# Kernel optimization log

Hardware: AMD Instinct MI355X
Metric: run time of the kernel (lower is better)

Reference implementation:

```python
import jax, jax.numpy as jnp
import numpy as np

N = 50000
E = 640000
IN_DIM = 23
HID = 128
NUM_CLASS = 12


def setup_inputs() -> dict:
    key = jax.random.key(0)
    ks = jax.random.split(key, 12)
    x = jax.random.normal(ks[0], (N, IN_DIM), dtype=jnp.float32)
    edge_index = jax.random.randint(ks[1], (2, E), 0, N, dtype=jnp.int32)

    def glorot(k, shape):
        fan_in, fan_out = shape
        lim = np.sqrt(6.0 / (fan_in + fan_out)).astype(np.float32)
        return jax.random.uniform(k, shape, jnp.float32, -lim, lim)

    W1 = glorot(ks[2], (IN_DIM, HID)); b1 = jnp.zeros((HID,), jnp.float32)
    W2 = glorot(ks[3], (HID, HID));    b2 = jnp.zeros((HID,), jnp.float32)
    W3 = glorot(ks[4], (HID, HID));    b3 = jnp.zeros((HID,), jnp.float32)
    Wc1 = glorot(ks[5], (HID, 64));    bc1 = jnp.zeros((64,), jnp.float32)
    Wc2 = glorot(ks[6], (64, NUM_CLASS)); bc2 = jnp.zeros((NUM_CLASS,), jnp.float32)
    return {"x": x, "edge_index": edge_index,
            "W1": W1, "b1": b1, "W2": W2, "b2": b2, "W3": W3, "b3": b3,
            "Wc1": Wc1, "bc1": bc1, "Wc2": Wc2, "bc2": bc2}


def _gcn_norm(edge_index, n_nodes):
    # add self loops, compute symmetric normalization D^-1/2 (A+I) D^-1/2
    loop = jnp.arange(n_nodes, dtype=edge_index.dtype)
    src = jnp.concatenate([edge_index[0], loop])
    dst = jnp.concatenate([edge_index[1], loop])
    deg = jax.ops.segment_sum(jnp.ones_like(dst, dtype=jnp.float32), dst,
                              num_segments=n_nodes)
    dinv = jax.lax.rsqrt(deg)  # deg >= 1 due to self loops
    norm = dinv[src] * dinv[dst]  # [E + N]
    return src, dst, norm


def _gcn_layer(h, W, b, src, dst, norm, n_nodes):
    h = h @ W                          # linear (bias applied after aggregation, per PyG)
    msg = h[src] * norm[:, None]       # gather + scale
    out = jax.ops.segment_sum(msg, dst, num_segments=n_nodes)  # scatter-add
    return out + b


def reference(x, edge_index, W1, b1, W2, b2, W3, b3, Wc1, bc1, Wc2, bc2):
    n = x.shape[0]
    src, dst, norm = _gcn_norm(edge_index, n)
    h = jnp.tanh(_gcn_layer(x, W1, b1, src, dst, norm, n))
    h = jnp.tanh(_gcn_layer(h, W2, b2, src, dst, norm, n))
    h = jnp.tanh(_gcn_layer(h, W3, b3, src, dst, norm, n))
    # dropout is identity in eval mode
    out = h @ Wc1 + bc1
    out = out @ Wc2 + bc2
    return out
```

## Files before the change

kernel.cpp:

```cpp
#include <hip/hip_runtime.h>
#include <math.h>

#define NN 50000
#define EE 640000
#define IND 23
#define HID 128
#define MIDD 64
#define NCLS 12
#define NB 49
#define QS 32766.0f
#define INVQS (1.0f / 32766.0f)
#define BSH 7
#define NBK 391
#define CHUNK 4096
#define NPB 157
#define PADB 6250
#define GB16 3125

typedef short short8v __attribute__((ext_vector_type(8)));
typedef float f32x4 __attribute__((ext_vector_type(4)));
typedef unsigned long long u64;

__device__ __forceinline__ short f2bf(float f) {
    unsigned u = __float_as_uint(f);
    unsigned r = (u + 0x7FFFu + ((u >> 16) & 1u)) >> 16;
    return (short)r;
}
__device__ __forceinline__ float bf2f(short s) {
    return __uint_as_float(((unsigned)(unsigned short)s) << 16);
}
__device__ __forceinline__ float fast_tanh(float x) {
    float t = __expf(-2.f * fabsf(x));
    float r = (1.f - t) / (1.f + t);
    return copysignf(r, x);
}

__global__ __launch_bounds__(256) void k_pre(const int* __restrict__ dst,
                                             int* __restrict__ cnt,
                                             const float* __restrict__ Wc1,
                                             const float* __restrict__ bc1,
                                             const float* __restrict__ Wc2,
                                             const float* __restrict__ bc2,
                                             float* __restrict__ Wcc,
                                             float* __restrict__ bcc,
                                             const float* __restrict__ W2,
                                             const float* __restrict__ W3,
                                             short* __restrict__ w2hi,
                                             short* __restrict__ w2lo,
                                             short* __restrict__ w3hi,
                                             short* __restrict__ w3lo) {
    const int bid = blockIdx.x;
    const int tid = threadIdx.x;
    if (bid < 2500) {
        int i = bid * 256 + tid;
        if (i < EE) atomicAdd(&cnt[dst[i]], 1);
        return;
    }
    if (bid < 2506) {
        int t = (bid - 2500) * 256 + tid;
        if (t < HID * NCLS) {
            int k = t / NCLS, c = t % NCLS;
            float s = 0.f;
#pragma unroll 8
            for (int j = 0; j < MIDD; ++j) s += Wc1[k * MIDD + j] * Wc2[j * NCLS + c];
            Wcc[t] = s;
        }
        if (t < NCLS) {
            float s = bc2[t];
#pragma unroll 8
            for (int j = 0; j < MIDD; ++j) s += bc1[j] * Wc2[j * NCLS + t];
            bcc[t] = s;
        }
        return;
    }
    int bb = bid - 2506;
    const float* W = (bb < 64) ? W2 : W3;
    short* hi = (bb < 64) ? w2hi : w3hi;
    short* lo = (bb < 64) ? w2lo : w3lo;
    int i = (bb & 63) * 256 + tid;
    int k = i >> 7, c = i & 127;
    float w = W[i];
    short h = f2bf(w);
    short l = f2bf(w - bf2f(h));
    hi[((k >> 3) * 128 + c) * 8 + (k & 7)] = h;
    lo[((k >> 3) * 128 + c) * 8 + (k & 7)] = l;
}

__global__ __launch_bounds__(256) void k_scan_local(const int* __restrict__ cnt,
                                                    int* __restrict__ row_ptr,
                                                    float* __restrict__ dinv,
                                                    int* __restrict__ sums) {
    __shared__ int wtot[4];
    const int tid = threadIdx.x;
    const int wid = tid >> 6, lane = tid & 63;
    const int base = blockIdx.x * 1024 + tid * 4;
    int v[4];
#pragma unroll
    for (int t = 0; t < 4; ++t) {
        int i = base + t;
        v[t] = (i < NN) ? cnt[i] : 0;
        if (i < NN) dinv[i] = rsqrtf((float)v[t] + 1.0f);
    }
    int slocal = v[0] + v[1] + v[2] + v[3];
    int val = slocal;
#pragma unroll
    for (int off = 1; off < 64; off <<= 1) {
        int t = __shfl_up(val, off, 64);
        if (lane >= off) val += t;
    }
    if (lane == 63) wtot[wid] = val;
    __syncthreads();
    int woff = 0;
#pragma unroll
    for (int w = 0; w < 4; ++w) woff += (w < wid) ? wtot[w] : 0;
    int run = woff + val - slocal;
#pragma unroll
    for (int t = 0; t < 4; ++t) {
        int i = base + t;
        if (i < NN) row_ptr[i] = run;
        run += v[t];
    }
    if (tid == 255) sums[blockIdx.x] = woff + val;
}

__global__ __launch_bounds__(256) void k_scan_apply2(int* __restrict__ row_ptr,
                                                     const int* __restrict__ sums,
                                                     int* __restrict__ bcurA) {
    __shared__ int so;
    const int tid = threadIdx.x;
    if (tid < 64) {
        int a = (tid < (int)blockIdx.x) ? sums[tid] : 0;
        int b = (tid < NB) ? sums[tid] : 0;
#pragma unroll
        for (int off = 32; off; off >>= 1) {
            a += __shfl_down(a, off, 64);
            b += __shfl_down(b, off, 64);
        }
        if (tid == 0) {
            so = a;
            if (blockIdx.x == NB - 1) row_ptr[NN] = b;
        }
    }
    __syncthreads();
    const int o = so;
    const int base = blockIdx.x * 1024 + tid * 4;
#pragma unroll
    for (int t = 0; t < 4; ++t) {
        int i = base + t;
        if (i < NN) {
            int rp = row_ptr[i] + o;
            row_ptr[i] = rp;
            if ((i & 127) == 0) bcurA[i >> BSH] = rp;
        }
    }
}

__global__ __launch_bounds__(256) void k_part(const int* __restrict__ src,
                                              const int* __restrict__ dst,
                                              const float* __restrict__ dinv,
                                              int* __restrict__ bcurA,
                                              u64* __restrict__ sw_g,
                                              int* __restrict__ d_g,
                                              const float* __restrict__ x,
                                              float* __restrict__ xp) {
    const int bid = blockIdx.x;
    const int tid = threadIdx.x;
    if (bid >= NPB) {
        int i = (bid - NPB) * 256 + tid;
        int node = i >> 5, f = i & 31;
        xp[i] = (f < IND) ? x[node * IND + f] * dinv[node] : 0.f;
        return;
    }
    __shared__ int hist[NBK], base[NBK], cur[NBK], gb[NBK];
    __shared__ u64 lsw[CHUNK];
    __shared__ int ld[CHUNK];
    const int e0 = bid * CHUNK;
    const int total = min(CHUNK, EE - e0);
    for (int t = tid; t < NBK; t += 256) hist[t] = 0;
    __syncthreads();
    int sv[16], dv[16];
#pragma unroll
    for (int t = 0; t < 16; ++t) {
        int i = e0 + t * 256 + tid;
        if (i < EE) {
            sv[t] = src[i];
            dv[t] = dst[i];
            atomicAdd(&hist[dv[t] >> BSH], 1);
        } else dv[t] = -1;
    }
    __syncthreads();
    if (tid < 64) {
        int carry = 0;
        for (int c = 0; c < NBK; c += 64) {
            int idx = c + tid;
            int v = (idx < NBK) ? hist[idx] : 0;
            int sc = v;
#pragma unroll
            for (int off = 1; off < 64; off <<= 1) {
                int tv = __shfl_up(sc, off, 64);
                if (tid >= off) sc += tv;
            }
            if (idx < NBK) base[idx] = carry + sc - v;
            carry += __shfl(sc, 63, 64);
        }
    }
    __syncthreads();
    for (int t = tid; t < NBK; t += 256) {
        cur[t] = base[t];
        gb[t] = hist[t] ? atomicAdd(&bcurA[t], hist[t]) : 0;
    }
    __syncthreads();
#pragma unroll
    for (int t = 0; t < 16; ++t) {
        if (dv[t] >= 0) {
            int b = dv[t] >> BSH;
            int r = atomicAdd(&cur[b], 1);
            lsw[r] = (unsigned)sv[t] |
                     ((u64)__float_as_uint(dinv[sv[t]]) << 32);
            ld[r] = dv[t];
        }
    }
    __syncthreads();
    for (int j = tid; j < total; j += 256) {
        int d = ld[j];
        int b = d >> BSH;
        int gpos = gb[b] + (j - base[b]);
        sw_g[gpos] = lsw[j];
        d_g[gpos] = d;
    }
}

__global__ __launch_bounds__(256) void k_sort(const int* __restrict__ row_ptr,
                                              const u64* __restrict__ sw_g,
                                              const int* __restrict__ d_g,
                                              u64* __restrict__ e_sn) {
    __shared__ int rloc[129];
    __shared__ int curl[128];
    __shared__ u64 osw[3072];
    const int bid = blockIdx.x, tid = threadIdx.x;
    const int n0 = bid << BSH;
    const int nlast = min(128, NN - n0);
    if (tid <= nlast) rloc[tid] = row_ptr[n0 + tid];
    if (tid < 128) curl[tid] = 0;
    __syncthreads();
    const int rbeg = rloc[0];
    const int cnt = rloc[nlast] - rbeg;
    for (int j = tid; j < cnt; j += 256) {
        int d = d_g[rbeg + j];
        int li = d - n0;
        int r = atomicAdd(&curl[li], 1);
        int pl = (rloc[li] - rbeg) + r;
        u64 v = sw_g[rbeg + j];
        if (pl < 3072) osw[pl] = v;
        else e_sn[rbeg + pl] = v;
    }
    __syncthreads();
    const int lim = min(cnt, 3072);
    for (int j = tid; j < lim; j += 256) e_sn[rbeg + j] = osw[j];
}

__global__ __launch_bounds__(256) void k_l1(const float* __restrict__ xp,
                                            const float* __restrict__ W1,
                                            const float* __restrict__ b1,
                                            const int* __restrict__ row_ptr,
                                            const int2* __restrict__ e_sn,
                                            const float* __restrict__ dinv,
                                            short* __restrict__ outq) {
    const int tid = threadIdx.x;
    const int i = blockIdx.x * 4 + (tid >> 6);
    const int lane = tid & 63;
    const int slot = lane >> 3;
    const int f = lane & 7;
    const float4* xp4 = (const float4*)xp;
    const int beg = row_ptr[i];
    const int deg = row_ptr[i + 1] - beg;
    float4 acc = make_float4(0.f, 0.f, 0.f, 0.f);
    for (int base = 0; base < deg; base += 64) {
        const int cnt = min(64, deg - base);
        int s_l = 0;
        if (lane < cnt) s_l = e_sn[beg + base + lane].x;
        int e = 0;
        for (; e + 8 <= cnt; e += 8) {
            int s = __shfl(s_l, e + slot, 64);
            float4 v = xp4[s * 8 + f];
            acc.x += v.x; acc.y += v.y; acc.z += v.z; acc.w += v.w;
        }
        if (e < cnt) {
            int s = __shfl(s_l, e + slot, 64);
            if (e + slot < cnt) {
                float4 v = xp4[s * 8 + f];
                acc.x += v.x; acc.y += v.y; acc.z += v.z; acc.w += v.w;
            }
        }
    }
#pragma unroll
    for (int off = 32; off >= 8; off >>= 1) {
        acc.x += __shfl_down(acc.x, off, 64);
        acc.y += __shfl_down(acc.y, off, 64);
        acc.z += __shfl_down(acc.z, off, 64);
        acc.w += __shfl_down(acc.w, off, 64);
    }
    const float di = dinv[i];
    if (lane < 8) {
        float4 v = xp4[i * 8 + lane];
        acc.x = (acc.x + v.x) * di; acc.y = (acc.y + v.y) * di;
        acc.z = (acc.z + v.z) * di; acc.w = (acc.w + v.w) * di;
    }
    float a0 = b1[lane], a1 = b1[lane + 64];
#pragma unroll
    for (int k = 0; k < IND; ++k) {
        float comp = ((k & 3) == 0) ? acc.x : ((k & 3) == 1) ? acc.y
                   : ((k & 3) == 2) ? acc.z : acc.w;
        float xk = __shfl(comp, k >> 2, 64);
        a0 += xk * W1[k * HID + lane];
        a1 += xk * W1[k * HID + lane + 64];
    }
    outq[i * HID + lane]      = (short)__float2int_rn(fast_tanh(a0) * QS);
    outq[i * HID + lane + 64] = (short)__float2int_rn(fast_tanh(a1) * QS);
}

__global__ __launch_bounds__(256) void k_aggq(const short* __restrict__ hq,
                                              const int* __restrict__ row_ptr,
                                              const int2* __restrict__ e_sn,
                                              const float* __restrict__ dinv,
                                              short8v* __restrict__ ah,
                                              short8v* __restrict__ al) {
    const int tid = threadIdx.x;
    const int i = blockIdx.x * 4 + (tid >> 6);
    const int lane = tid & 63;
    const int slot = lane >> 4;
    const int f = lane & 15;
    const short8v* h8 = (const short8v*)hq;
    const int beg = row_ptr[i];
    const int deg = row_ptr[i + 1] - beg;
    float facc[8];
#pragma unroll
    for (int t = 0; t < 8; ++t) facc[t] = 0.f;
    for (int base = 0; base < deg; base += 64) {
        const int cnt = min(64, deg - base);
        int s_l = 0; float n_l = 0.f;
        if (lane < cnt) {
            int2 sn = e_sn[beg + base + lane];
            s_l = sn.x;
            n_l = __int_as_float(sn.y);
        }
        int e = 0;
#pragma unroll 4
        for (; e + 4 <= cnt; e += 4) {
            int s = __shfl(s_l, e + slot, 64);
            float nr = __shfl(n_l, e + slot, 64);
            short8v v = h8[(size_t)s * 16 + f];
#pragma unroll
            for (int t = 0; t < 8; ++t) facc[t] += (float)v[t] * nr;
        }
        if (e < cnt) {
            int s = __shfl(s_l, e + slot, 64);
            float nr = __shfl(n_l, e + slot, 64);
            if (e + slot < cnt) {
                short8v v = h8[(size_t)s * 16 + f];
#pragma unroll
                for (int t = 0; t < 8; ++t) facc[t] += (float)v[t] * nr;
            }
        }
    }
#pragma unroll
    for (int off = 32; off >= 16; off >>= 1)
#pragma unroll
        for (int t = 0; t < 8; ++t) facc[t] += __shfl_down(facc[t], off, 64);
    if (lane < 16) {
        const float di = dinv[i];
        const float sc = di * INVQS;
        short8v v = h8[(size_t)i * 16 + lane];
        short8v hi8, lo8;
#pragma unroll
        for (int t = 0; t < 8; ++t) {
            float o = (facc[t] + di * (float)v[t]) * sc;
            short h = f2bf(o);
            hi8[t] = h;
            lo8[t] = f2bf(o - bf2f(h));
        }
        ah[(size_t)i * 16 + lane] = hi8;
        al[(size_t)i * 16 + lane] = lo8;
    }
}

#define GEMM_CORE16                                                            \
    const int tid = threadIdx.x;                                               \
    const int lane = tid & 63, wv = tid >> 6;                                  \
    const int g = lane >> 4, c16 = lane & 15;                                  \
    const int rb = blockIdx.x * 16;                                            \
    const int colb = wv * 32;                                                  \
    const size_t arow = (size_t)(rb + c16) * 16;                               \
    short8v Ah[4], Al[4], Bh[4][2], Bl[4][2];                                  \
    _Pragma("unroll")                                                          \
    for (int t = 0; t < 4; ++t) {                                              \
        Ah[t] = ah[arow + t * 4 + g];                                          \
        Al[t] = al[arow + t * 4 + g];                                          \
        _Pragma("unroll")                                                      \
        for (int ct = 0; ct < 2; ++ct) {                                       \
            int wi = (t * 4 + g) * 128 + colb + ct * 16 + c16;                 \
            Bh[t][ct] = whi8[wi];                                              \
            Bl[t][ct] = wlo8[wi];                                              \
        }                                                                      \
    }                                                                          \
    __builtin_amdgcn_sched_barrier(0);                                         \
    f32x4 acc[2];                                                              \
    acc[0] = f32x4{0.f, 0.f, 0.f, 0.f};                                        \
    acc[1] = f32x4{0.f, 0.f, 0.f, 0.f};                                        \
    _Pragma("unroll")                                                          \
    for (int t = 0; t < 4; ++t) {                                              \
        _Pragma("unroll")                                                      \
        for (int ct = 0; ct < 2; ++ct) {                                       \
            acc[ct] = __builtin_amdgcn_mfma_f32_16x16x32_bf16(Ah[t], Bh[t][ct], acc[ct], 0, 0, 0); \
            acc[ct] = __builtin_amdgcn_mfma_f32_16x16x32_bf16(Ah[t], Bl[t][ct], acc[ct], 0, 0, 0); \
            acc[ct] = __builtin_amdgcn_mfma_f32_16x16x32_bf16(Al[t], Bh[t][ct], acc[ct], 0, 0, 0); \
        }                                                                      \
    }

__global__ __launch_bounds__(256) void k_gemm_q(const short8v* __restrict__ ah,
                                                const short8v* __restrict__ al,
                                                const short8v* __restrict__ whi8,
                                                const short8v* __restrict__ wlo8,
                                                const float* __restrict__ bias,
                                                short* __restrict__ qout) {
    GEMM_CORE16
#pragma unroll
    for (int ct = 0; ct < 2; ++ct) {
        const int col = colb + ct * 16 + c16;
        const float bb = bias[col];
#pragma unroll
        for (int r = 0; r < 4; ++r) {
            int nd = rb + 4 * g + r;
            float v = fast_tanh(acc[ct][r] + bb);
            qout[nd * HID + col] = (short)__float2int_rn(v * QS);
        }
    }
}

__global__ __launch_bounds__(256) void k_gemm_head(const short8v* __restrict__ ah,
                                                   const short8v* __restrict__ al,
                                                   const short8v* __restrict__ whi8,
                                                   const short8v* __restrict__ wlo8,
                                                   const float* __restrict__ bias,
                                                   const float* __restrict__ Wcc,
                                                   const float* __restrict__ bcc,
                                                   float* __restrict__ outp) {
    __shared__ float WccS[HID * NCLS];
    __shared__ float bccS[NCLS];
    __shared__ float psum[4][16][NCLS];
    {
        const int t0 = threadIdx.x;
        for (int t = t0; t < HID * NCLS; t += 256) WccS[t] = Wcc[t];
        if (t0 < NCLS) bccS[t0] = bcc[t0];
    }
    __syncthreads();
    GEMM_CORE16
    float part[4][NCLS];
#pragma unroll
    for (int r = 0; r < 4; ++r)
#pragma unroll
        for (int c = 0; c < NCLS; ++c) part[r][c] = 0.f;
#pragma unroll
    for (int ct = 0; ct < 2; ++ct) {
        const int col = colb + ct * 16 + c16;
        const float bb = bias[col];
        const float4* wr = (const float4*)&WccS[col * NCLS];
        float4 wa = wr[0], wb2 = wr[1], wc = wr[2];
#pragma unroll
        for (int r = 0; r < 4; ++r) {
            float v = fast_tanh(acc[ct][r] + bb);
            part[r][0]  += v * wa.x;  part[r][1]  += v * wa.y;
            part[r][2]  += v * wa.z;  part[r][3]  += v * wa.w;
            part[r][4]  += v * wb2.x; part[r][5]  += v * wb2.y;
            part[r][6]  += v * wb2.z; part[r][7]  += v * wb2.w;
            part[r][8]  += v * wc.x;  part[r][9]  += v * wc.y;
            part[r][10] += v * wc.z;  part[r][11] += v * wc.w;
        }
    }
#pragma unroll
    for (int off = 8; off; off >>= 1)
#pragma unroll
        for (int r = 0; r < 4; ++r)
#pragma unroll
            for (int c = 0; c < NCLS; ++c)
                part[r][c] += __shfl_down(part[r][c], off, 64);
    if (c16 == 0) {
#pragma unroll
        for (int r = 0; r < 4; ++r)
#pragma unroll
            for (int c = 0; c < NCLS; ++c)
                psum[wv][4 * g + r][c] = part[r][c];
    }
    __syncthreads();
    if (tid < 16 * NCLS) {
        int row = tid / NCLS, c = tid % NCLS;
        float s = bccS[c] + psum[0][row][c] + psum[1][row][c]
                + psum[2][row][c] + psum[3][row][c];
        outp[(rb + row) * NCLS + c] = s;
    }
}


extern "C" void kernel_launch(void* const* d_in, const int* in_sizes, int n_in,
                              void* d_out, int out_size, void* d_ws, size_t ws_size,
                              hipStream_t stream) {
    const float* x    = (const float*)d_in[0];
    const int*   edge = (const int*)d_in[1];
    const int*   src  = edge;
    const int*   dst  = edge + EE;
    const float* W1  = (const float*)d_in[2];  const float* b1  = (const float*)d_in[3];
    const float* W2  = (const float*)d_in[4];  const float* b2  = (const float*)d_in[5];
    const float* W3  = (const float*)d_in[6];  const float* b3  = (const float*)d_in[7];
    const float* Wc1 = (const float*)d_in[8];  const float* bc1 = (const float*)d_in[9];
    const float* Wc2 = (const float*)d_in[10]; const float* bc2 = (const float*)d_in[11];
    float* outp = (float*)d_out;

    char* p = (char*)d_ws;
    int*   cnt     = (int*)p;   p += 200064;
    int*   row_ptr = (int*)p;   p += 200064;
    float* dinv    = (float*)p; p += 200064;
    int*   sums    = (int*)p;   p += 256;
    int*   bcurA   = (int*)p;   p += 2048;
    int2*  e_sn    = (int2*)p;  p += (size_t)EE * 8;
    u64*   sw_g    = (u64*)p;   p += (size_t)EE * 8;
    int*   d_g     = (int*)p;   p += (size_t)EE * 4;
    float* xp      = (float*)p; p += (size_t)NN * 32 * 4;
    short* q       = (short*)p; p += (size_t)NN * HID * 2;
    short8v* ah    = (short8v*)p; p += (size_t)(NN + 16) * 256;
    short8v* al    = (short8v*)p; p += (size_t)(NN + 16) * 256;
    float* Wcc     = (float*)p; p += HID * NCLS * 4;
    float* bcc     = (float*)p; p += 256;
    short* w2hi    = (short*)p; p += 32768;
    short* w2lo    = (short*)p; p += 32768;
    short* w3hi    = (short*)p; p += 32768;
    short* w3lo    = (short*)p; p += 32768;

    hipMemsetAsync(cnt, 0, (size_t)NN * 4, stream);
    k_pre        <<<2634, 256, 0, stream>>>(dst, cnt, Wc1, bc1, Wc2, bc2, Wcc, bcc,
                                            W2, W3, w2hi, w2lo, w3hi, w3lo);
    k_scan_local <<<NB, 256, 0, stream>>>(cnt, row_ptr, dinv, sums);
    k_scan_apply2<<<NB, 256, 0, stream>>>(row_ptr, sums, bcurA);
    k_part       <<<NPB + PADB, 256, 0, stream>>>(src, dst, dinv, bcurA,
                                                  sw_g, d_g, x, xp);
    k_sort       <<<NBK, 256, 0, stream>>>(row_ptr, sw_g, d_g, (u64*)e_sn);

    k_l1  <<<NN / 4, 256, 0, stream>>>(xp, W1, b1, row_ptr, e_sn, dinv, q);
    k_aggq     <<<NN / 4, 256, 0, stream>>>(q, row_ptr, e_sn, dinv, ah, al);
    k_gemm_q   <<<GB16, 256, 0, stream>>>(ah, al, (const short8v*)w2hi,
                                          (const short8v*)w2lo, b2, q);
    k_aggq     <<<NN / 4, 256, 0, stream>>>(q, row_ptr, e_sn, dinv, ah, al);
    k_gemm_head<<<GB16, 256, 0, stream>>>(ah, al, (const short8v*)w3hi,
                                          (const short8v*)w3lo, b3, Wcc, bcc, outp);
}
```

Before: 289.5 us.

## Split layer-1 into aggregation kernel and split-bf16 MFMA GEMM kernel

Layer 1 used to aggregate raw features and then do the 23x128 matmul with scalar FMAs and shuffles inside the same kernel. It is now split into an aggregation kernel that writes hi/lo bf16 halves of the aggregated features, plus a new MFMA kernel. That kernel runs a three-term split-bf16 16x16x32 GEMM against a pre-packed, zero-padded W1 and applies bias, tanh and quantization. This moves the layer-1 matmul onto matrix cores, at the cost of an extra launch, an intermediate buffer round-trip, and extra W1 packing blocks in the pre-kernel.

```diff
diff --git a/kernel.cpp b/kernel.cpp
--- a/kernel.cpp
+++ b/kernel.cpp
@@ -18,6 +18,7 @@
 #define GB16 3125
 
 typedef short short8v __attribute__((ext_vector_type(8)));
+typedef short short4v __attribute__((ext_vector_type(4)));
 typedef float f32x4 __attribute__((ext_vector_type(4)));
 typedef unsigned long long u64;
 
@@ -48,7 +49,10 @@
                                              short* __restrict__ w2hi,
                                              short* __restrict__ w2lo,
                                              short* __restrict__ w3hi,
-                                             short* __restrict__ w3lo) {
+                                             short* __restrict__ w3lo,
+                                             const float* __restrict__ W1,
+                                             short* __restrict__ w1hi,
+                                             short* __restrict__ w1lo) {
     const int bid = blockIdx.x;
     const int tid = threadIdx.x;
     if (bid < 2500) {
@@ -73,17 +77,27 @@
         }
         return;
     }
-    int bb = bid - 2506;
-    const float* W = (bb < 64) ? W2 : W3;
-    short* hi = (bb < 64) ? w2hi : w3hi;
-    short* lo = (bb < 64) ? w2lo : w3lo;
-    int i = (bb & 63) * 256 + tid;
+    if (bid < 2634) {
+        int bb = bid - 2506;
+        const float* W = (bb < 64) ? W2 : W3;
+        short* hi = (bb < 64) ? w2hi : w3hi;
+        short* lo = (bb < 64) ? w2lo : w3lo;
+        int i = (bb & 63) * 256 + tid;
+        int k = i >> 7, c = i & 127;
+        float w = W[i];
+        short h = f2bf(w);
+        short l = f2bf(w - bf2f(h));
+        hi[((k >> 3) * 128 + c) * 8 + (k & 7)] = h;
+        lo[((k >> 3) * 128 + c) * 8 + (k & 7)] = l;
+        return;
+    }
+    int i = (bid - 2634) * 256 + tid;
     int k = i >> 7, c = i & 127;
-    float w = W[i];
+    float w = (k < IND) ? W1[k * HID + c] : 0.f;
     short h = f2bf(w);
     short l = f2bf(w - bf2f(h));
-    hi[((k >> 3) * 128 + c) * 8 + (k & 7)] = h;
-    lo[((k >> 3) * 128 + c) * 8 + (k & 7)] = l;
+    w1hi[((k >> 3) * 128 + c) * 8 + (k & 7)] = h;
+    w1lo[((k >> 3) * 128 + c) * 8 + (k & 7)] = l;
 }
 
 __global__ __launch_bounds__(256) void k_scan_local(const int* __restrict__ cnt,
@@ -259,13 +273,12 @@
     for (int j = tid; j < lim; j += 256) e_sn[rbeg + j] = osw[j];
 }
 
-__global__ __launch_bounds__(256) void k_l1(const float* __restrict__ xp,
-                                            const float* __restrict__ W1,
-                                            const float* __restrict__ b1,
-                                            const int* __restrict__ row_ptr,
-                                            const int2* __restrict__ e_sn,
-                                            const float* __restrict__ dinv,
-                                            short* __restrict__ outq) {
+__global__ __launch_bounds__(256) void k_aggx(const float* __restrict__ xp,
+                                              const int* __restrict__ row_ptr,
+                                              const int2* __restrict__ e_sn,
+                                              const float* __restrict__ dinv,
+                                              short4v* __restrict__ axh,
+                                              short4v* __restrict__ axl) {
     const int tid = threadIdx.x;
     const int i = blockIdx.x * 4 + (tid >> 6);
     const int lane = tid & 63;
@@ -300,23 +313,65 @@
         acc.z += __shfl_down(acc.z, off, 64);
         acc.w += __shfl_down(acc.w, off, 64);
     }
-    const float di = dinv[i];
     if (lane < 8) {
+        const float di = dinv[i];
         float4 v = xp4[i * 8 + lane];
-        acc.x = (acc.x + v.x) * di; acc.y = (acc.y + v.y) * di;
-        acc.z = (acc.z + v.z) * di; acc.w = (acc.w + v.w) * di;
-    }
-    float a0 = b1[lane], a1 = b1[lane + 64];
-#pragma unroll
-    for (int k = 0; k < IND; ++k) {
-        float comp = ((k & 3) == 0) ? acc.x : ((k & 3) == 1) ? acc.y
-                   : ((k & 3) == 2) ? acc.z : acc.w;
-        float xk = __shfl(comp, k >> 2, 64);
-        a0 += xk * W1[k * HID + lane];
-        a1 += xk * W1[k * HID + lane + 64];
-    }
-    outq[i * HID + lane]      = (short)__float2int_rn(fast_tanh(a0) * QS);
-    outq[i * HID + lane + 64] = (short)__float2int_rn(fast_tanh(a1) * QS);
+        float a[4];
+        a[0] = (acc.x + v.x) * di; a[1] = (acc.y + v.y) * di;
+        a[2] = (acc.z + v.z) * di; a[3] = (acc.w + v.w) * di;
+        short4v h4, l4;
+#pragma unroll
+        for (int j = 0; j < 4; ++j) {
+            short h = f2bf(a[j]);
+            h4[j] = h;
+            l4[j] = f2bf(a[j] - bf2f(h));
+        }
+        axh[(size_t)i * 8 + lane] = h4;
+        axl[(size_t)i * 8 + lane] = l4;
+    }
+}
+
+__global__ __launch_bounds__(256) void k_gemm_l1(const short8v* __restrict__ axh8,
+                                                 const short8v* __restrict__ axl8,
+                                                 const short8v* __restrict__ w1hi8,
+                                                 const short8v* __restrict__ w1lo8,
+                                                 const float* __restrict__ bias,
+                                                 short* __restrict__ qout) {
+    const int tid = threadIdx.x;
+    const int lane = tid & 63, wv = tid >> 6;
+    const int g = lane >> 4, c16 = lane & 15;
+    const int rb = blockIdx.x * 16;
+    const int colb = wv * 32;
+    short8v Ah = axh8[(size_t)(rb + c16) * 4 + g];
+    short8v Al = axl8[(size_t)(rb + c16) * 4 + g];
+    short8v Bh[2], Bl[2];
+#pragma unroll
+    for (int ct = 0; ct < 2; ++ct) {
+        int wi = g * 128 + colb + ct * 16 + c16;
+        Bh[ct] = w1hi8[wi];
+        Bl[ct] = w1lo8[wi];
+    }
+    __builtin_amdgcn_sched_barrier(0);
+    f32x4 acc[2];
+    acc[0] = f32x4{0.f, 0.f, 0.f, 0.f};
+    acc[1] = f32x4{0.f, 0.f, 0.f, 0.f};
+#pragma unroll
+    for (int ct = 0; ct < 2; ++ct) {
+        acc[ct] = __builtin_amdgcn_mfma_f32_16x16x32_bf16(Ah, Bh[ct], acc[ct], 0, 0, 0);
+        acc[ct] = __builtin_amdgcn_mfma_f32_16x16x32_bf16(Ah, Bl[ct], acc[ct], 0, 0, 0);
+        acc[ct] = __builtin_amdgcn_mfma_f32_16x16x32_bf16(Al, Bh[ct], acc[ct], 0, 0, 0);
+    }
+#pragma unroll
+    for (int ct = 0; ct < 2; ++ct) {
+        const int col = colb + ct * 16 + c16;
+        const float bb = bias[col];
+#pragma unroll
+        for (int r = 0; r < 4; ++r) {
+            int nd = rb + 4 * g + r;
+            float v = fast_tanh(acc[ct][r] + bb);
+            qout[nd * HID + col] = (short)__float2int_rn(v * QS);
+        }
+    }
 }
 
 __global__ __launch_bounds__(256) void k_aggq(const short* __restrict__ hq,
@@ -528,23 +583,31 @@
     short* q       = (short*)p; p += (size_t)NN * HID * 2;
     short8v* ah    = (short8v*)p; p += (size_t)(NN + 16) * 256;
     short8v* al    = (short8v*)p; p += (size_t)(NN + 16) * 256;
+    short4v* axh   = (short4v*)p; p += (size_t)(NN + 16) * 64;
+    short4v* axl   = (short4v*)p; p += (size_t)(NN + 16) * 64;
     float* Wcc     = (float*)p; p += HID * NCLS * 4;
     float* bcc     = (float*)p; p += 256;
     short* w2hi    = (short*)p; p += 32768;
     short* w2lo    = (short*)p; p += 32768;
     short* w3hi    = (short*)p; p += 32768;
     short* w3lo    = (short*)p; p += 32768;
+    short* w1hi    = (short*)p; p += 8192;
+    short* w1lo    = (short*)p; p += 8192;
 
     hipMemsetAsync(cnt, 0, (size_t)NN * 4, stream);
-    k_pre        <<<2634, 256, 0, stream>>>(dst, cnt, Wc1, bc1, Wc2, bc2, Wcc, bcc,
-                                            W2, W3, w2hi, w2lo, w3hi, w3lo);
+    k_pre        <<<2650, 256, 0, stream>>>(dst, cnt, Wc1, bc1, Wc2, bc2, Wcc, bcc,
+                                            W2, W3, w2hi, w2lo, w3hi, w3lo,
+                                            W1, w1hi, w1lo);
     k_scan_local <<<NB, 256, 0, stream>>>(cnt, row_ptr, dinv, sums);
     k_scan_apply2<<<NB, 256, 0, stream>>>(row_ptr, sums, bcurA);
     k_part       <<<NPB + PADB, 256, 0, stream>>>(src, dst, dinv, bcurA,
                                                   sw_g, d_g, x, xp);
     k_sort       <<<NBK, 256, 0, stream>>>(row_ptr, sw_g, d_g, (u64*)e_sn);
 
-    k_l1  <<<NN / 4, 256, 0, stream>>>(xp, W1, b1, row_ptr, e_sn, dinv, q);
+    k_aggx    <<<NN / 4, 256, 0, stream>>>(xp, row_ptr, e_sn, dinv, axh, axl);
+    k_gemm_l1 <<<GB16, 256, 0, stream>>>((const short8v*)axh, (const short8v*)axl,
+                                         (const short8v*)w1hi, (const short8v*)w1lo,
+                                         b1, q);
     k_aggq     <<<NN / 4, 256, 0, stream>>>(q, row_ptr, e_sn, dinv, ah, al);
     k_gemm_q   <<<GB16, 256, 0, stream>>>(ah, al, (const short8v*)w2hi,
                                           (const short8v*)w2lo, b2, q);
```

Measured after the change: 288.4 us (median of 2 runs). About the same (-0.4%).
